# Kernel tuning notes

Measured on AMD Instinct MI355X. Metric: run time of the kernel, lower is better.

The kernel has to match this reference:

```python
import jax, jax.numpy as jnp
import numpy as np

N = 200000   # nodes
R = 4        # relations
E = 1000000  # edges per relation
B = 1024     # graphs in batch


def _graph_conv(h, s, d, ew, W, b):
    """DGL GraphConv, norm='both', optional edge_weight. h:[N,F_in] -> [N,F_out]."""
    n = h.shape[0]
    ones = jnp.ones(s.shape[0], dtype=h.dtype)
    out_deg = jnp.clip(jax.ops.segment_sum(ones, s, num_segments=n), 1.0)
    in_deg = jnp.clip(jax.ops.segment_sum(ones, d, num_segments=n), 1.0)
    hs = h * jax.lax.rsqrt(out_deg)[:, None]          # src-side norm
    m = hs[s]                                         # gather: [E, F_in]
    if ew is not None:
        m = m * ew[:, None]
    agg = jax.ops.segment_sum(m, d, num_segments=n)   # scatter-sum: [N, F_in]
    rst = agg * jax.lax.rsqrt(in_deg)[:, None]        # dst-side norm
    return rst @ W + b


def _hetero_layer(h, src, dst, ew, W, b):
    out = None
    for r in range(R):
        ewr = None if ew is None else ew[r]
        o = _graph_conv(h, src[r], dst[r], ewr, W[r], b[r])
        out = o if out is None else out + o
    return out


def setup_inputs() -> dict:
    key = jax.random.key(0)
    ks = jax.random.split(key, 10)
    feat = jax.random.normal(ks[0], (N, 2), dtype=jnp.float32)
    src = jax.random.randint(ks[1], (R, E), 0, N, dtype=jnp.int32)
    dst = jax.random.randint(ks[2], (R, E), 0, N, dtype=jnp.int32)
    ew = jax.random.uniform(ks[3], (R, E), dtype=jnp.float32)
    graph_ids = jnp.sort(jax.random.randint(ks[4], (N,), 0, B, dtype=jnp.int32))
    W1 = jax.random.normal(ks[5], (R, 2, 16), dtype=jnp.float32) * 0.5
    b1 = jnp.zeros((R, 16), dtype=jnp.float32)
    W2 = jax.random.normal(ks[6], (R, 16, 16), dtype=jnp.float32) * 0.25
    b2 = jnp.zeros((R, 16), dtype=jnp.float32)
    Wc = jax.random.normal(ks[7], (16, 2), dtype=jnp.float32) * 0.25
    bc = jnp.zeros((2,), dtype=jnp.float32)
    return {"feat": feat, "src": src, "dst": dst, "ew": ew,
            "graph_ids": graph_ids, "W1": W1, "b1": b1,
            "W2": W2, "b2": b2, "Wc": Wc, "bc": bc}


def reference(feat, src, dst, ew, graph_ids, W1, b1, W2, b2, Wc, bc):
    # layer 1: per-relation weighted GraphConv, summed over relations
    h = _hetero_layer(feat, src, dst, ew, W1, b1)
    h = jax.nn.relu(h)
    # layer 2: no edge weights (kwargs not forwarded in original code)
    h = _hetero_layer(h, src, dst, None, W2, b2)
    # mean_nodes per graph in the batch
    sums = jax.ops.segment_sum(h, graph_ids, num_segments=B)          # [B,16]
    cnts = jax.ops.segment_sum(jnp.ones((N,), h.dtype), graph_ids, num_segments=B)
    hg = sums / jnp.clip(cnts, 1.0)[:, None]
    return hg @ Wc + bc                                               # [B,2]
```

## Files before the change

kernel.cpp:

```cpp
#include <hip/hip_runtime.h>
#include <hip/hip_fp16.h>

#define NN 200000
#define RR 4
#define EE 1000000
#define BB 1024
#define RN (RR*NN)

#define BSH 7
#define BSZ 128
#define NB 1563
#define RK (RR*NB)
#define CSH 10
#define CNODES 1024
#define CC 196
#define CAPC 5632
#define EPB 8192
#define SBT 1024
#define BPR ((EE + EPB - 1) / EPB)
#define GSLOTS 32
#define CAPB 896

#define SRC_OF(u)  (((u) >> 7) & 0x3FFFF)
#define DL_OF(u)   ((int)((u) & 127))
#define DEG_OF(u)  ((u) >> 25)

#define OFF_POOL   0
#define OFF_CNT    (OFF_POOL + BB*16)
#define OFF_GCS    (OFF_CNT + BB)
#define OFF_GCD    (OFF_GCS + RR*CC)
#define OFF_GFIN   (OFF_GCD + RR*CC)
#define ZERO_UNITS (OFF_GFIN + RK)
#define OFF_DEGB   ZERO_UNITS
#define OFF_INVI   (OFF_DEGB + RN/4)
#define OFF_RW16   (OFF_INVI + RN)
#define OFF_AGG1   (OFF_RW16 + RN/2)
#define OFF_SBC    OFF_AGG1
#define OFF_H1H    (OFF_AGG1 + RN*2)
#define OFF_KWCL   (OFF_H1H + NN*8)
#define OFF_KWCE   (OFF_KWCL + RR*CC*CAPC)
#define OFF_KW4    (OFF_KWCE + RR*CC*CAPC/2)


__global__ __launch_bounds__(SBT) void k_part(const int* __restrict__ src,
                                              const int* __restrict__ dst,
                                              const float* __restrict__ ew,
                                              int* __restrict__ gcs,
                                              int* __restrict__ gcd,
                                              unsigned short* __restrict__ sbc,
                                              unsigned* __restrict__ kwcL,
                                              unsigned short* __restrict__ kwcE) {
  __shared__ int cS[CC], bS[CC], lS[CC];
  __shared__ int cD[CC], bD[CC], lD[CC];
  int t = threadIdx.x, r = blockIdx.y, c0 = blockIdx.x * EPB;
  if (t < CC) { cS[t] = 0; cD[t] = 0; }
  __syncthreads();
  for (int i = t; i < EPB; i += SBT) {
    int e = c0 + i;
    if (e < EE) {
      atomicAdd(&cS[src[r * EE + e] >> CSH], 1);
      atomicAdd(&cD[dst[r * EE + e] >> CSH], 1);
    }
  }
  __syncthreads();
  if (t < CC) {
    int v = cS[t]; bS[t] = v ? atomicAdd(&gcs[r * CC + t], v) : 0; lS[t] = 0;
    int w = cD[t]; bD[t] = w ? atomicAdd(&gcd[r * CC + t], w) : 0; lD[t] = 0;
  }
  __syncthreads();
  for (int i = t; i < EPB; i += SBT) {
    int e = c0 + i;
    if (e < EE) {
      int idx = r * EE + e;
      int s = src[idx], d = dst[idx];
      int cs = s >> CSH;
      int offs = bS[cs] + atomicAdd(&lS[cs], 1);
      if (offs < CAPC)
        sbc[(size_t)(r * CC + cs) * CAPC + offs] = (unsigned short)(s & (CNODES - 1));
      int cd = d >> CSH;
      int offd = bD[cd] + atomicAdd(&lD[cd], 1);
      if (offd < CAPC) {
        size_t stD = (size_t)(r * CC + cd) * CAPC;
        kwcL[stD + offd] = (unsigned)(d & (CNODES - 1)) | ((unsigned)s << CSH);
        kwcE[stD + offd] = __half_as_ushort(__float2half_rn(ew[idx]));
      }
    }
  }
}

__global__ __launch_bounds__(1024) void k_fineS(const unsigned short* __restrict__ sbc,
                                                const int* __restrict__ gcs,
                                                unsigned char* __restrict__ degb) {
  __shared__ int h[CNODES];
  int t = threadIdx.x, c = blockIdx.x, r = blockIdx.y;
  int kc = r * CC + c;
  size_t st = (size_t)kc * CAPC;
  int m = min(gcs[kc], CAPC);
  h[t] = 0;
  __syncthreads();
  for (int i = t; i < m; i += 1024) atomicAdd(&h[sbc[st + i]], 1);
  __syncthreads();
  int n = c * CNODES + t;
  if (n < NN) degb[r * NN + n] = (unsigned char)min(max(h[t], 1), 63);
}

__global__ __launch_bounds__(1024) void k_fineD(const unsigned* __restrict__ kwcL,
                                                const unsigned short* __restrict__ kwcE,
                                                const int* __restrict__ gcd,
                                                const unsigned char* __restrict__ degb,
                                                const float* __restrict__ feat,
                                                unsigned* __restrict__ kw4,
                                                int* __restrict__ gfin,
                                                float* __restrict__ invi,
                                                unsigned short* __restrict__ rw16,
                                                float* __restrict__ agg1) {
  __shared__ int h[CNODES];
  __shared__ float la[CNODES * 2];
  __shared__ int s4[1024];
  __shared__ int sfb[9];
  int t = threadIdx.x, c = blockIdx.x, r = blockIdx.y;
  int kc = r * CC + c;
  size_t stc = (size_t)kc * CAPC;
  int nrec = min(gcd[kc], CAPC);
  h[t] = 0; la[t] = 0.f; la[t + CNODES] = 0.f;
  __syncthreads();
  for (int i = t; i < nrec; i += 1024) atomicAdd(&h[kwcL[stc + i] & (CNODES - 1)], 1);
  __syncthreads();
  int cntt = h[t];
  s4[t] = cntt;
  __syncthreads();
  for (int off = 1; off < 1024; off <<= 1) {
    int v = (t >= off) ? s4[t - off] : 0;
    __syncthreads();
    s4[t] += v;
    __syncthreads();
  }
  int base = s4[t] - cntt;
  if ((t & 127) == 0) sfb[t >> 7] = base;
  if (t == 1023) sfb[8] = s4[1023];
  __syncthreads();
  int n0 = c * CNODES;
  {
    int sb = sfb[t >> 7];
    int n = n0 + t;
    if (n < NN) {
      invi[r * NN + n] = rsqrtf((float)max(cntt, 1));
      rw16[r * NN + n] = (unsigned short)min(base - sb, CAPB);
    }
  }
  if (t < 8) {
    int kb = c * 8 + t;
    if (kb < NB) gfin[r * NB + kb] = min(sfb[t + 1] - sfb[t], CAPB);
  }
  __syncthreads();
  h[t] = base;
  __syncthreads();
  for (int i = t; i < nrec; i += 1024) {
    unsigned rc = kwcL[stc + i];
    int dcl = rc & (CNODES - 1);
    int s = rc >> CSH;
    float ewf = __half2float(__ushort_as_half(kwcE[stc + i]));
    unsigned dg = degb[r * NN + s];
    float w1 = ewf * rsqrtf((float)dg);
    float2 fv = ((const float2*)feat)[s];
    atomicAdd(&la[dcl * 2],     fv.x * w1);
    atomicAdd(&la[dcl * 2 + 1], fv.y * w1);
    int pos = atomicAdd(&h[dcl], 1);
    int fb = dcl >> 7;
    int fpos = pos - sfb[fb];
    if (fpos < CAPB)
      kw4[(size_t)(r * NB + c * 8 + fb) * CAPB + fpos] =
          (rc & 127u) | ((unsigned)s << 7) | (dg << 25);
  }
  __syncthreads();
  {
    int n = n0 + t;
    if (n < NN)
      ((float2*)agg1)[r * NN + n] = make_float2(la[t * 2], la[t * 2 + 1]);
  }
}

__device__ __forceinline__ unsigned pack2h(float a, float b) {
  __half2 h = __floats2half2_rn(a, b);
  return *reinterpret_cast<unsigned*>(&h);
}

__global__ __launch_bounds__(256) void k_l1b(const float* __restrict__ agg1,
                                             const float* __restrict__ invi,
                                             const float* __restrict__ W1,
                                             const float* __restrict__ b1,
                                             __half* __restrict__ h1h) {
  __shared__ float sW[RR * 2 * 16];
  __shared__ float sb[16];
  int t = threadIdx.x, b = blockIdx.x;
  if (t < RR * 2 * 16) sW[t] = W1[t];
  if (t < 16) {
    float s = 0.f;
    for (int r = 0; r < RR; r++) s += b1[r * 16 + t];
    sb[t] = s;
  }
  __syncthreads();
  int n = b * 256 + t;
  if (n >= NN) return;
  float acc[16];
#pragma unroll
  for (int j = 0; j < 16; j++) acc[j] = sb[j];
#pragma unroll
  for (int r = 0; r < RR; r++) {
    float iv = invi[r * NN + n];
    float2 a = ((const float2*)agg1)[r * NN + n];
    float a0 = a.x * iv, a1 = a.y * iv;
#pragma unroll
    for (int j = 0; j < 16; j++)
      acc[j] += a0 * sW[(r * 2 + 0) * 16 + j] + a1 * sW[(r * 2 + 1) * 16 + j];
  }
#pragma unroll
  for (int j = 0; j < 16; j++) acc[j] = fmaxf(acc[j], 0.f);
  uint4 u0, u1;
  u0.x = pack2h(acc[0], acc[1]);  u0.y = pack2h(acc[2], acc[3]);
  u0.z = pack2h(acc[4], acc[5]);  u0.w = pack2h(acc[6], acc[7]);
  u1.x = pack2h(acc[8], acc[9]);  u1.y = pack2h(acc[10], acc[11]);
  u1.z = pack2h(acc[12], acc[13]); u1.w = pack2h(acc[14], acc[15]);
  uint4* o = (uint4*)(h1h + (size_t)n * 16);
  o[0] = u0; o[1] = u1;
}

__device__ __forceinline__ void acc8(float* acc, uint4 u, float w) {
  float2 p;
  p = __half22float2(*(__half2*)&u.x); acc[0] += p.x * w; acc[1] += p.y * w;
  p = __half22float2(*(__half2*)&u.y); acc[2] += p.x * w; acc[3] += p.y * w;
  p = __half22float2(*(__half2*)&u.z); acc[4] += p.x * w; acc[5] += p.y * w;
  p = __half22float2(*(__half2*)&u.w); acc[6] += p.x * w; acc[7] += p.y * w;
}

__global__ __launch_bounds__(256) void k_l2(const unsigned* __restrict__ kw4,
                                            const int* __restrict__ gfin,
                                            const unsigned short* __restrict__ rw16,
                                            const __half* __restrict__ h1h,
                                            const float* __restrict__ invi,
                                            const float* __restrict__ W2,
                                            const int* __restrict__ gid,
                                            float* __restrict__ pool,
                                            float* __restrict__ cnt) {
  __shared__ float agg[BSZ * 17];
  __shared__ float sW[16 * 16];
  __shared__ int   sg[BSZ];
  __shared__ unsigned short srw[BSZ + 1];
  __shared__ float gslot[GSLOTS * 16];
  __shared__ int   cslot[GSLOTS];
  __shared__ int   present[GSLOTS];
  int t = threadIdx.x, b = blockIdx.x, r = blockIdx.y;
  int n0 = b << BSH;
  int k = r * NB + b;
  int m = min(gfin[k], CAPB);
  sW[t] = W2[r * 256 + t];
  if (t < GSLOTS) { cslot[t] = 0; present[t] = 0; }
  for (int i = t; i < GSLOTS * 16; i += 256) gslot[i] = 0.f;
  if (t < BSZ) {
    int n = n0 + t;
    srw[t] = (n < NN) ? rw16[r * NN + n] : (unsigned short)m;
  }
  if (t == BSZ) srw[BSZ] = (unsigned short)m;
  __syncthreads();
  const uint4* h4p = (const uint4*)h1h;
  const unsigned* rb = kw4 + (size_t)k * CAPB;
  int f8 = t & 1, g = t >> 1;
  int e = srw[g], en = srw[g + 1];
  float acc[8];
#pragma unroll
  for (int j = 0; j < 8; j++) acc[j] = 0.f;
  for (; e + 3 < en; e += 4) {
    unsigned r0 = rb[e], r1 = rb[e + 1], r2 = rb[e + 2], r3 = rb[e + 3];
    uint4 u0 = h4p[(size_t)SRC_OF(r0) * 2 + f8];
    uint4 u1 = h4p[(size_t)SRC_OF(r1) * 2 + f8];
    uint4 u2 = h4p[(size_t)SRC_OF(r2) * 2 + f8];
    uint4 u3 = h4p[(size_t)SRC_OF(r3) * 2 + f8];
    acc8(acc, u0, rsqrtf((float)DEG_OF(r0)));
    acc8(acc, u1, rsqrtf((float)DEG_OF(r1)));
    acc8(acc, u2, rsqrtf((float)DEG_OF(r2)));
    acc8(acc, u3, rsqrtf((float)DEG_OF(r3)));
  }
  for (; e < en; e++) {
    unsigned rr = rb[e];
    uint4 u = h4p[(size_t)SRC_OF(rr) * 2 + f8];
    acc8(acc, u, rsqrtf((float)DEG_OF(rr)));
  }
#pragma unroll
  for (int j = 0; j < 8; j++) agg[g * 17 + 8 * f8 + j] = acc[j];
  __syncthreads();
  int n = n0 + t;
  int g0 = gid[n0];
  bool valid = (t < BSZ) && (n < NN);
  float out[16];
#pragma unroll
  for (int j = 0; j < 16; j++) out[j] = 0.f;
  if (valid) {
    float iv = invi[r * NN + n];
#pragma unroll
    for (int kk = 0; kk < 16; kk++) {
      float a = agg[t * 17 + kk] * iv;
#pragma unroll
      for (int j = 0; j < 16; j++) out[j] += a * sW[kk * 16 + j];
    }
  }
  __syncthreads();
  if (t < BSZ) {
    sg[t] = valid ? (gid[n] - g0) : -1;
#pragma unroll
    for (int j = 0; j < 16; j++) agg[t * 17 + j] = out[j];
  }
  __syncthreads();
  {
    int f = t & 15, i0 = t >> 4;
    for (int i = i0; i < BSZ; i += 16) {
      int gsN = sg[i];
      if (gsN < 0) continue;
      float v = agg[i * 17 + f];
      if (gsN < GSLOTS) {
        atomicAdd(&gslot[gsN * 16 + f], v);
        if (f == 0) {
          present[gsN] = 1;
          if (r == 0) atomicAdd(&cslot[gsN], 1);
        }
      } else {
        atomicAdd(&pool[(g0 + gsN) * 16 + f], v);
        if (f == 0 && r == 0) atomicAdd(&cnt[g0 + gsN], 1.0f);
      }
    }
  }
  __syncthreads();
  if (t < GSLOTS * 16) {
    int gsN = t >> 4, f = t & 15;
    if (present[gsN]) atomicAdd(&pool[(g0 + gsN) * 16 + f], gslot[t]);
  }
  if (r == 0 && t < GSLOTS && cslot[t] > 0)
    atomicAdd(&cnt[g0 + t], (float)cslot[t]);
}

__global__ __launch_bounds__(256) void k_final(const float* __restrict__ pool,
                                               const float* __restrict__ cnt,
                                               const float* __restrict__ b2,
                                               const float* __restrict__ Wc,
                                               const float* __restrict__ bc,
                                               float* __restrict__ out) {
  int b = blockIdx.x * 256 + threadIdx.x;
  if (b >= BB) return;
  float c = cnt[b];
  float inv = 1.0f / fmaxf(c, 1.0f);
  float o0 = bc[0], o1 = bc[1];
#pragma unroll
  for (int j = 0; j < 16; j++) {
    float sb = 0.f;
    for (int r = 0; r < RR; r++) sb += b2[r * 16 + j];
    float v = (pool[b * 16 + j] + c * sb) * inv;
    o0 += v * Wc[j * 2 + 0];
    o1 += v * Wc[j * 2 + 1];
  }
  out[b * 2 + 0] = o0;
  out[b * 2 + 1] = o1;
}

extern "C" void kernel_launch(void* const* d_in, const int* in_sizes, int n_in,
                              void* d_out, int out_size, void* d_ws, size_t ws_size,
                              hipStream_t stream) {
  const float* feat = (const float*)d_in[0];
  const int*   src  = (const int*)d_in[1];
  const int*   dst  = (const int*)d_in[2];
  const float* ew   = (const float*)d_in[3];
  const int*   gid  = (const int*)d_in[4];
  const float* W1   = (const float*)d_in[5];
  const float* b1   = (const float*)d_in[6];
  const float* W2   = (const float*)d_in[7];
  const float* b2   = (const float*)d_in[8];
  const float* Wc   = (const float*)d_in[9];
  const float* bc   = (const float*)d_in[10];

  char* ws = (char*)d_ws;
  float* pool   = (float*)(ws + (size_t)OFF_POOL * 4);
  float* cnt    = (float*)(ws + (size_t)OFF_CNT  * 4);
  int*   gcs    = (int*)  (ws + (size_t)OFF_GCS  * 4);
  int*   gcd    = (int*)  (ws + (size_t)OFF_GCD  * 4);
  int*   gfin   = (int*)  (ws + (size_t)OFF_GFIN * 4);
  unsigned char*  degb = (unsigned char*) (ws + (size_t)OFF_DEGB * 4);
  float* invi   = (float*)(ws + (size_t)OFF_INVI * 4);
  unsigned short* rw16 = (unsigned short*)(ws + (size_t)OFF_RW16 * 4);
  float* agg1   = (float*)(ws + (size_t)OFF_AGG1 * 4);
  unsigned short* sbc  = (unsigned short*)(ws + (size_t)OFF_SBC * 4);
  __half* h1h   = (__half*)(ws + (size_t)OFF_H1H * 4);
  unsigned* kwcL = (unsigned*)(ws + (size_t)OFF_KWCL * 4);
  unsigned short* kwcE = (unsigned short*)(ws + (size_t)OFF_KWCE * 4);
  unsigned* kw4 = (unsigned*)(ws + (size_t)OFF_KW4 * 4);

  hipMemsetAsync(d_ws, 0, (size_t)ZERO_UNITS * 4, stream);

  k_part  <<<dim3(BPR, RR), SBT, 0, stream>>>(src, dst, ew, gcs, gcd, sbc, kwcL, kwcE);
  k_fineS <<<dim3(CC, RR), 1024, 0, stream>>>(sbc, gcs, degb);
  k_fineD <<<dim3(CC, RR), 1024, 0, stream>>>(kwcL, kwcE, gcd, degb, feat, kw4, gfin, invi, rw16, agg1);
  k_l1b   <<<(NN + 255) / 256, 256, 0, stream>>>(agg1, invi, W1, b1, h1h);
  k_l2    <<<dim3(NB, RR), 256, 0, stream>>>(kw4, gfin, rw16, h1h, invi, W2, gid, pool, cnt);
  k_final <<<(BB + 255) / 256, 256, 0, stream>>>(pool, cnt, b2, Wc, bc, (float*)d_out);
}
```

Measured before the change: 351.9 us.

## Replace fixed-capacity bucket buffers with exact prefix-summed compact edge layout

Adds a counting pass and a single-block scan so each coarse bucket gets an exact offset, instead of fixed-capacity slots that could silently drop overflowing edges. Destination records are packed into one 64-bit word (index plus half-precision weight) rather than two separate arrays. The fine-bucket records for layer 2 are also written compactly, with offsets carried through gfin. This removes the capacity clamps and makes memory use dense, at the cost of an extra full read of src/dst and two more launches.

```diff
diff --git a/kernel.cpp b/kernel.cpp
--- a/kernel.cpp
+++ b/kernel.cpp
@@ -14,42 +14,108 @@
 #define CSH 10
 #define CNODES 1024
 #define CC 196
-#define CAPC 5632
 #define EPB 8192
 #define SBT 1024
 #define BPR ((EE + EPB - 1) / EPB)
 #define GSLOTS 32
-#define CAPB 896
 
 #define SRC_OF(u)  (((u) >> 7) & 0x3FFFF)
 #define DL_OF(u)   ((int)((u) & 127))
 #define DEG_OF(u)  ((u) >> 25)
 
-#define OFF_POOL   0
-#define OFF_CNT    (OFF_POOL + BB*16)
-#define OFF_GCS    (OFF_CNT + BB)
-#define OFF_GCD    (OFF_GCS + RR*CC)
-#define OFF_GFIN   (OFF_GCD + RR*CC)
-#define ZERO_UNITS (OFF_GFIN + RK)
-#define OFF_DEGB   ZERO_UNITS
-#define OFF_INVI   (OFF_DEGB + RN/4)
-#define OFF_RW16   (OFF_INVI + RN)
-#define OFF_AGG1   (OFF_RW16 + RN/2)
-#define OFF_SBC    OFF_AGG1
-#define OFF_H1H    (OFF_AGG1 + RN*2)
-#define OFF_KWCL   (OFF_H1H + NN*8)
-#define OFF_KWCE   (OFF_KWCL + RR*CC*CAPC)
-#define OFF_KW4    (OFF_KWCE + RR*CC*CAPC/2)
-
+#define OFF_POOL    0
+#define OFF_CNT     (OFF_POOL + BB*16)
+#define OFF_CNTS    (OFF_CNT + BB)
+#define OFF_CNTD    (OFF_CNTS + RR*CC)
+#define OFF_CURS    (OFF_CNTD + RR*CC)
+#define OFF_CURD    (OFF_CURS + RR*CC)
+#define OFF_GSB     (OFF_CURD + RR*CC)
+#define OFF_GDB     (OFF_GSB + RR*CC + 1)
+#define OFF_GFIN    (OFF_GDB + RR*CC + 1)
+#define ZERO_UNITS_ (OFF_GFIN + RK + 1)
+#define ZERO_UNITS  (ZERO_UNITS_ + (ZERO_UNITS_ & 1))
+#define OFF_DEGB    ZERO_UNITS
+#define OFF_INVI    (OFF_DEGB + RN/4)
+#define OFF_RW16    (OFF_INVI + RN)
+#define OFF_AGG1    (OFF_RW16 + RN/2)
+#define OFF_SBC     OFF_AGG1
+#define OFF_H1H     (OFF_AGG1 + RN*2)
+#define OFF_KWC_    (OFF_H1H + NN*8)
+#define OFF_KWC     (OFF_KWC_ + (OFF_KWC_ & 1))
+#define OFF_KW4     (OFF_KWC + RR*EE*2)
+
+
+__global__ __launch_bounds__(1024) void k_cnt(const int* __restrict__ src,
+                                              const int* __restrict__ dst,
+                                              int* __restrict__ cntS,
+                                              int* __restrict__ cntD) {
+  __shared__ int hS[CC], hD[CC];
+  int t = threadIdx.x, r = blockIdx.y, c0 = blockIdx.x * EPB;
+  if (t < CC) { hS[t] = 0; hD[t] = 0; }
+  __syncthreads();
+  for (int i = t; i < EPB; i += 1024) {
+    int e = c0 + i;
+    if (e < EE) {
+      atomicAdd(&hS[src[r * EE + e] >> CSH], 1);
+      atomicAdd(&hD[dst[r * EE + e] >> CSH], 1);
+    }
+  }
+  __syncthreads();
+  if (t < CC) {
+    if (hS[t]) atomicAdd(&cntS[r * CC + t], hS[t]);
+    if (hD[t]) atomicAdd(&cntD[r * CC + t], hD[t]);
+  }
+}
+
+__global__ __launch_bounds__(1024) void k_scan(const int* __restrict__ cntS,
+                                               const int* __restrict__ cntD,
+                                               int* __restrict__ gsb,
+                                               int* __restrict__ gdb,
+                                               int* __restrict__ gfin) {
+  __shared__ int s[1024];
+  int t = threadIdx.x;
+  int v = (t < RR * CC) ? cntS[t] : 0;
+  s[t] = v;
+  __syncthreads();
+  for (int off = 1; off < 1024; off <<= 1) {
+    int u = (t >= off) ? s[t - off] : 0;
+    __syncthreads();
+    s[t] += u;
+    __syncthreads();
+  }
+  if (t < RR * CC) {
+    int r = t / CC;
+    int pre = (r == 0) ? 0 : s[r * CC - 1];
+    gsb[t] = r * EE + (s[t] - v) - pre;
+  }
+  if (t == 0) gsb[RR * CC] = RR * EE;
+  __syncthreads();
+  int w = (t < RR * CC) ? cntD[t] : 0;
+  s[t] = w;
+  __syncthreads();
+  for (int off = 1; off < 1024; off <<= 1) {
+    int u = (t >= off) ? s[t - off] : 0;
+    __syncthreads();
+    s[t] += u;
+    __syncthreads();
+  }
+  if (t < RR * CC) {
+    int r = t / CC;
+    int pre = (r == 0) ? 0 : s[r * CC - 1];
+    gdb[t] = r * EE + (s[t] - w) - pre;
+  }
+  if (t == 0) { gdb[RR * CC] = RR * EE; gfin[RK] = RR * EE; }
+}
 
 __global__ __launch_bounds__(SBT) void k_part(const int* __restrict__ src,
                                               const int* __restrict__ dst,
                                               const float* __restrict__ ew,
-                                              int* __restrict__ gcs,
-                                              int* __restrict__ gcd,
+                                              const int* __restrict__ gsb,
+                                              const int* __restrict__ gdb,
+                                              int* __restrict__ curS,
+                                              int* __restrict__ curD,
                                               unsigned short* __restrict__ sbc,
-                                              unsigned* __restrict__ kwcL,
-                                              unsigned short* __restrict__ kwcE) {
+                                              unsigned long long* __restrict__ kwc) {
   __shared__ int cS[CC], bS[CC], lS[CC];
   __shared__ int cD[CC], bD[CC], lD[CC];
   int t = threadIdx.x, r = blockIdx.y, c0 = blockIdx.x * EPB;
@@ -64,8 +130,9 @@
   }
   __syncthreads();
   if (t < CC) {
-    int v = cS[t]; bS[t] = v ? atomicAdd(&gcs[r * CC + t], v) : 0; lS[t] = 0;
-    int w = cD[t]; bD[t] = w ? atomicAdd(&gcd[r * CC + t], w) : 0; lD[t] = 0;
+    int kc = r * CC + t;
+    int v = cS[t]; bS[t] = v ? gsb[kc] + atomicAdd(&curS[kc], v) : 0; lS[t] = 0;
+    int w = cD[t]; bD[t] = w ? gdb[kc] + atomicAdd(&curD[kc], w) : 0; lD[t] = 0;
   }
   __syncthreads();
   for (int i = t; i < EPB; i += SBT) {
@@ -74,39 +141,34 @@
       int idx = r * EE + e;
       int s = src[idx], d = dst[idx];
       int cs = s >> CSH;
-      int offs = bS[cs] + atomicAdd(&lS[cs], 1);
-      if (offs < CAPC)
-        sbc[(size_t)(r * CC + cs) * CAPC + offs] = (unsigned short)(s & (CNODES - 1));
+      sbc[(size_t)bS[cs] + atomicAdd(&lS[cs], 1)] = (unsigned short)(s & (CNODES - 1));
       int cd = d >> CSH;
-      int offd = bD[cd] + atomicAdd(&lD[cd], 1);
-      if (offd < CAPC) {
-        size_t stD = (size_t)(r * CC + cd) * CAPC;
-        kwcL[stD + offd] = (unsigned)(d & (CNODES - 1)) | ((unsigned)s << CSH);
-        kwcE[stD + offd] = __half_as_ushort(__float2half_rn(ew[idx]));
-      }
+      unsigned low = (unsigned)(d & (CNODES - 1)) | ((unsigned)s << CSH);
+      unsigned long long rec =
+          ((unsigned long long)__half_as_ushort(__float2half_rn(ew[idx])) << 32) | low;
+      kwc[(size_t)bD[cd] + atomicAdd(&lD[cd], 1)] = rec;
     }
   }
 }
 
 __global__ __launch_bounds__(1024) void k_fineS(const unsigned short* __restrict__ sbc,
-                                                const int* __restrict__ gcs,
+                                                const int* __restrict__ gsb,
                                                 unsigned char* __restrict__ degb) {
   __shared__ int h[CNODES];
   int t = threadIdx.x, c = blockIdx.x, r = blockIdx.y;
   int kc = r * CC + c;
-  size_t st = (size_t)kc * CAPC;
-  int m = min(gcs[kc], CAPC);
+  int s0 = gsb[kc];
+  int m = gsb[kc + 1] - s0;
   h[t] = 0;
   __syncthreads();
-  for (int i = t; i < m; i += 1024) atomicAdd(&h[sbc[st + i]], 1);
+  for (int i = t; i < m; i += 1024) atomicAdd(&h[sbc[(size_t)s0 + i]], 1);
   __syncthreads();
   int n = c * CNODES + t;
   if (n < NN) degb[r * NN + n] = (unsigned char)min(max(h[t], 1), 63);
 }
 
-__global__ __launch_bounds__(1024) void k_fineD(const unsigned* __restrict__ kwcL,
-                                                const unsigned short* __restrict__ kwcE,
-                                                const int* __restrict__ gcd,
+__global__ __launch_bounds__(1024) void k_fineD(const unsigned long long* __restrict__ kwc,
+                                                const int* __restrict__ gdb,
                                                 const unsigned char* __restrict__ degb,
                                                 const float* __restrict__ feat,
                                                 unsigned* __restrict__ kw4,
@@ -117,14 +179,15 @@
   __shared__ int h[CNODES];
   __shared__ float la[CNODES * 2];
   __shared__ int s4[1024];
-  __shared__ int sfb[9];
+  __shared__ int sfb[8];
   int t = threadIdx.x, c = blockIdx.x, r = blockIdx.y;
   int kc = r * CC + c;
-  size_t stc = (size_t)kc * CAPC;
-  int nrec = min(gcd[kc], CAPC);
+  int b0 = gdb[kc];
+  int nrec = gdb[kc + 1] - b0;
   h[t] = 0; la[t] = 0.f; la[t + CNODES] = 0.f;
   __syncthreads();
-  for (int i = t; i < nrec; i += 1024) atomicAdd(&h[kwcL[stc + i] & (CNODES - 1)], 1);
+  for (int i = t; i < nrec; i += 1024)
+    atomicAdd(&h[(unsigned)kwc[(size_t)b0 + i] & (CNODES - 1)], 1);
   __syncthreads();
   int cntt = h[t];
   s4[t] = cntt;
@@ -137,40 +200,35 @@
   }
   int base = s4[t] - cntt;
   if ((t & 127) == 0) sfb[t >> 7] = base;
-  if (t == 1023) sfb[8] = s4[1023];
   __syncthreads();
   int n0 = c * CNODES;
   {
-    int sb = sfb[t >> 7];
     int n = n0 + t;
     if (n < NN) {
       invi[r * NN + n] = rsqrtf((float)max(cntt, 1));
-      rw16[r * NN + n] = (unsigned short)min(base - sb, CAPB);
+      rw16[r * NN + n] = (unsigned short)(base - sfb[t >> 7]);
     }
   }
   if (t < 8) {
     int kb = c * 8 + t;
-    if (kb < NB) gfin[r * NB + kb] = min(sfb[t + 1] - sfb[t], CAPB);
+    if (kb < NB) gfin[r * NB + kb] = b0 + sfb[t];
   }
   __syncthreads();
   h[t] = base;
   __syncthreads();
   for (int i = t; i < nrec; i += 1024) {
-    unsigned rc = kwcL[stc + i];
-    int dcl = rc & (CNODES - 1);
-    int s = rc >> CSH;
-    float ewf = __half2float(__ushort_as_half(kwcE[stc + i]));
+    unsigned long long rc = kwc[(size_t)b0 + i];
+    unsigned low = (unsigned)rc;
+    int dcl = low & (CNODES - 1);
+    int s = low >> CSH;
+    float ewf = __half2float(__ushort_as_half((unsigned short)(rc >> 32)));
     unsigned dg = degb[r * NN + s];
     float w1 = ewf * rsqrtf((float)dg);
     float2 fv = ((const float2*)feat)[s];
     atomicAdd(&la[dcl * 2],     fv.x * w1);
     atomicAdd(&la[dcl * 2 + 1], fv.y * w1);
     int pos = atomicAdd(&h[dcl], 1);
-    int fb = dcl >> 7;
-    int fpos = pos - sfb[fb];
-    if (fpos < CAPB)
-      kw4[(size_t)(r * NB + c * 8 + fb) * CAPB + fpos] =
-          (rc & 127u) | ((unsigned)s << 7) | (dg << 25);
+    kw4[(size_t)b0 + pos] = ((unsigned)dcl & 127u) | ((unsigned)s << 7) | (dg << 25);
   }
   __syncthreads();
   {
@@ -252,7 +310,8 @@
   int t = threadIdx.x, b = blockIdx.x, r = blockIdx.y;
   int n0 = b << BSH;
   int k = r * NB + b;
-  int m = min(gfin[k], CAPB);
+  int base = gfin[k];
+  int m = gfin[k + 1] - base;
   sW[t] = W2[r * 256 + t];
   if (t < GSLOTS) { cslot[t] = 0; present[t] = 0; }
   for (int i = t; i < GSLOTS * 16; i += 256) gslot[i] = 0.f;
@@ -263,7 +322,7 @@
   if (t == BSZ) srw[BSZ] = (unsigned short)m;
   __syncthreads();
   const uint4* h4p = (const uint4*)h1h;
-  const unsigned* rb = kw4 + (size_t)k * CAPB;
+  const unsigned* rb = kw4 + (size_t)base;
   int f8 = t & 1, g = t >> 1;
   int e = srw[g], en = srw[g + 1];
   float acc[8];
@@ -378,8 +437,12 @@
   char* ws = (char*)d_ws;
   float* pool   = (float*)(ws + (size_t)OFF_POOL * 4);
   float* cnt    = (float*)(ws + (size_t)OFF_CNT  * 4);
-  int*   gcs    = (int*)  (ws + (size_t)OFF_GCS  * 4);
-  int*   gcd    = (int*)  (ws + (size_t)OFF_GCD  * 4);
+  int*   cntS   = (int*)  (ws + (size_t)OFF_CNTS * 4);
+  int*   cntD   = (int*)  (ws + (size_t)OFF_CNTD * 4);
+  int*   curS   = (int*)  (ws + (size_t)OFF_CURS * 4);
+  int*   curD   = (int*)  (ws + (size_t)OFF_CURD * 4);
+  int*   gsb    = (int*)  (ws + (size_t)OFF_GSB  * 4);
+  int*   gdb    = (int*)  (ws + (size_t)OFF_GDB  * 4);
   int*   gfin   = (int*)  (ws + (size_t)OFF_GFIN * 4);
   unsigned char*  degb = (unsigned char*) (ws + (size_t)OFF_DEGB * 4);
   float* invi   = (float*)(ws + (size_t)OFF_INVI * 4);
@@ -387,15 +450,16 @@
   float* agg1   = (float*)(ws + (size_t)OFF_AGG1 * 4);
   unsigned short* sbc  = (unsigned short*)(ws + (size_t)OFF_SBC * 4);
   __half* h1h   = (__half*)(ws + (size_t)OFF_H1H * 4);
-  unsigned* kwcL = (unsigned*)(ws + (size_t)OFF_KWCL * 4);
-  unsigned short* kwcE = (unsigned short*)(ws + (size_t)OFF_KWCE * 4);
+  unsigned long long* kwc = (unsigned long long*)(ws + (size_t)OFF_KWC * 4);
   unsigned* kw4 = (unsigned*)(ws + (size_t)OFF_KW4 * 4);
 
   hipMemsetAsync(d_ws, 0, (size_t)ZERO_UNITS * 4, stream);
 
-  k_part  <<<dim3(BPR, RR), SBT, 0, stream>>>(src, dst, ew, gcs, gcd, sbc, kwcL, kwcE);
-  k_fineS <<<dim3(CC, RR), 1024, 0, stream>>>(sbc, gcs, degb);
-  k_fineD <<<dim3(CC, RR), 1024, 0, stream>>>(kwcL, kwcE, gcd, degb, feat, kw4, gfin, invi, rw16, agg1);
+  k_cnt   <<<dim3(BPR, RR), 1024, 0, stream>>>(src, dst, cntS, cntD);
+  k_scan  <<<1, 1024, 0, stream>>>(cntS, cntD, gsb, gdb, gfin);
+  k_part  <<<dim3(BPR, RR), SBT, 0, stream>>>(src, dst, ew, gsb, gdb, curS, curD, sbc, kwc);
+  k_fineS <<<dim3(CC, RR), 1024, 0, stream>>>(sbc, gsb, degb);
+  k_fineD <<<dim3(CC, RR), 1024, 0, stream>>>(kwc, gdb, degb, feat, kw4, gfin, invi, rw16, agg1);
   k_l1b   <<<(NN + 255) / 256, 256, 0, stream>>>(agg1, invi, W1, b1, h1h);
   k_l2    <<<dim3(NB, RR), 256, 0, stream>>>(kw4, gfin, rw16, h1h, invi, W2, gid, pool, cnt);
   k_final <<<(BB + 255) / 256, 256, 0, stream>>>(pool, cnt, b2, Wc, bc, (float*)d_out);
```

After: 340.9 us. -3.1%, faster.
